# Kernel optimization log

Measured on AMD Instinct MI355X. Metric: run time of the kernel, lower is better.

Reference implementation:

```python
import jax, jax.numpy as jnp
import numpy as np


def _resize_bilinear_ac(x, Ht, Wt):
    # bilinear resize with align_corners=True; x: [B,C,h,w] -> [B,C,Ht,Wt]
    B, C, h, w = x.shape
    ys = jnp.linspace(0.0, h - 1.0, Ht)
    xs = jnp.linspace(0.0, w - 1.0, Wt)
    y0 = jnp.floor(ys).astype(jnp.int32)
    y1 = jnp.minimum(y0 + 1, h - 1)
    x0 = jnp.floor(xs).astype(jnp.int32)
    x1 = jnp.minimum(x0 + 1, w - 1)
    wy = (ys - y0).astype(x.dtype)[None, None, :, None]
    wx = (xs - x0).astype(x.dtype)[None, None, None, :]
    r0 = x[:, :, y0, :]
    r1 = x[:, :, y1, :]
    v00 = r0[:, :, :, x0]; v01 = r0[:, :, :, x1]
    v10 = r1[:, :, :, x0]; v11 = r1[:, :, :, x1]
    return (1 - wy) * ((1 - wx) * v00 + wx * v01) + wy * ((1 - wx) * v10 + wx * v11)


def _grid_sample_zeros_ac(img, grid):
    # F.grid_sample(mode='bilinear', padding_mode='zeros', align_corners=True)
    # img: [B,C,H,W], grid: [B,H,W,2] in [-1,1] (x, y)
    B, C, H, W = img.shape
    x = (grid[..., 0] + 1.0) * 0.5 * (W - 1)  # [B,H,W] pixel coords
    y = (grid[..., 1] + 1.0) * 0.5 * (H - 1)
    x0 = jnp.floor(x)
    y0 = jnp.floor(y)
    wx = (x - x0)[:, None]  # [B,1,H,W]
    wy = (y - y0)[:, None]

    def gather(xi, yi):
        valid = ((xi >= 0) & (xi <= W - 1) & (yi >= 0) & (yi <= H - 1)).astype(img.dtype)
        xc = jnp.clip(xi, 0, W - 1).astype(jnp.int32)
        yc = jnp.clip(yi, 0, H - 1).astype(jnp.int32)
        v = jax.vmap(lambda im, yy, xx: im[:, yy, xx])(img, yc, xc)  # [B,C,H,W]
        return v * valid[:, None]

    v00 = gather(x0, y0)
    v01 = gather(x0 + 1, y0)
    v10 = gather(x0, y0 + 1)
    v11 = gather(x0 + 1, y0 + 1)
    return (1 - wy) * ((1 - wx) * v00 + wx * v01) + wy * ((1 - wx) * v10 + wx * v11)


def setup_inputs() -> dict:
    key = jax.random.key(0)
    k1, k2, k3 = jax.random.split(key, 3)
    B, C, H, W = 8, 3, 384, 1280
    h, w = 96, 320
    image = jax.random.normal(k1, (B, C, H, W), dtype=jnp.float32)
    # positive disparity (fraction of width, scaled by W inside forward)
    disp = jax.random.uniform(k2, (B, 1, h, w), dtype=jnp.float32, minval=0.01, maxval=0.3)
    scene = jax.random.normal(k3, (B, 3, h, w), dtype=jnp.float32) * 0.1
    K = jnp.array([[371.0, 0.0, 320.0], [0.0, 371.0, 96.0], [0.0, 0.0, 1.0]], dtype=jnp.float32)
    intrinsic = jnp.tile(K[None], (B, 1, 1))
    aug_size = jnp.tile(jnp.array([192.0, 640.0], dtype=jnp.float32)[None], (B, 1))
    return {"image": image, "disp": disp, "scene": scene, "intrinsic": intrinsic, "aug_size": aug_size}


def reference(image, disp, scene, intrinsic, aug_size):
    B, C, H, W = image.shape
    # interpolate_as(disp, image) * W
    disp_full = _resize_bilinear_ac(disp, H, W) * W
    # rel_scale = local_scale / aug_size, local_scale = (H, W)
    rel = jnp.array([H, W], dtype=aug_size.dtype) / aug_size  # [B,2] = (sy, sx)
    sy, sx = rel[:, 0], rel[:, 1]
    fx = intrinsic[:, 0, 0] * sx
    fy = intrinsic[:, 1, 1] * sy
    cx = intrinsic[:, 0, 2] * sx
    cy = intrinsic[:, 1, 2] * sy
    z = jnp.zeros_like(fx)
    o = jnp.ones_like(fx)
    K = jnp.stack([jnp.stack([fx, z, cx], 1),
                   jnp.stack([z, fy, cy], 1),
                   jnp.stack([z, z, o], 1)], 1)  # [B,3,3]
    # disp2depth_stereo_clamp
    depth = jnp.clip(fx[:, None, None, None] * 0.54 / (disp_full + 1e-8), 0.001, 80.0)
    # pixel2point
    xg, yg = jnp.meshgrid(jnp.arange(W, dtype=jnp.float32), jnp.arange(H, dtype=jnp.float32))  # [H,W]
    pix = jnp.stack([xg.ravel(), yg.ravel(), jnp.ones(H * W, dtype=jnp.float32)], 0)  # [3,HW]
    Kinv = jnp.linalg.inv(K)
    point = jnp.einsum('bij,jn->bin', Kinv, pix) * depth.reshape(B, 1, -1)  # [B,3,HW]
    # point2pixel_ms
    scene_full = _resize_bilinear_ac(scene, H, W)
    point_form = point.reshape(B, 3, H, W) + scene_full
    proj = jnp.einsum('bij,bjn->bin', K, point_form.reshape(B, 3, -1))
    coord = (proj[:, 0:2] / (proj[:, 2:3] + 1e-8)).reshape(B, 2, H, W)
    nx = coord[:, 0] / (W - 1) * 2.0 - 1.0
    ny = coord[:, 1] / (H - 1) * 2.0 - 1.0
    grid = jnp.stack([nx, ny], -1)  # [B,H,W,2]
    return _grid_sample_zeros_ac(image, grid)
```

## Files before the change

### kernel.cpp

```cpp
#include <hip/hip_runtime.h>
#include <hip/hip_fp16.h>

#define BATCH 8
#define CH 3
#define H_OUT 384
#define W_OUT 1280
#define H_IN 96
#define W_IN 320
#define HW_OUT (H_OUT * W_OUT)
#define HW_IN (H_IN * W_IN)

#define XS_PER_ROW 20
#define YSEGS (H_OUT / 4)
#define CHUNKS_PER_B (YSEGS * XS_PER_ROW)

#define LCOLS 18
#define LROWS 3

#define P1STRIDE 1282
#define P1_HALVES ((size_t)(1 + (size_t)BATCH * H_OUT * P1STRIDE) * 4)
#define P1_BYTES (P1_HALVES * 2)

struct __attribute__((packed, aligned(4))) f2 { float x, y; };
struct __attribute__((packed, aligned(8))) h8 { unsigned int w[4]; };

static __device__ __forceinline__ __half2 u2h2(unsigned int u) {
    return *reinterpret_cast<__half2*>(&u);
}

__global__ __launch_bounds__(256) void pack_single_kernel(
    const float* __restrict__ image, __half* __restrict__ pk)
{
    int i = blockIdx.x * 256 + threadIdx.x;
    int b = i / HW_OUT;
    int p = i - b * HW_OUT;
    int y = p / W_OUT;
    int x = p - y * W_OUT;
    const float* ib = image + (size_t)b * (CH * HW_OUT) + p;
    __half2 lo = __floats2half2_rn(ib[0], ib[HW_OUT]);
    __half2 hi = __floats2half2_rn(ib[2 * HW_OUT], 0.0f);
    uint2 v;
    v.x = *reinterpret_cast<unsigned int*>(&lo);
    v.y = *reinterpret_cast<unsigned int*>(&hi);
    __half* pd = pk + 4;
    size_t row = (size_t)b * H_OUT + y;
    *reinterpret_cast<uint2*>(pd + (row * P1STRIDE + x) * 4) = v;
    if (i < BATCH * H_OUT) {
        uint2 z; z.x = 0u; z.y = 0u;
        size_t r = (size_t)i;
        *reinterpret_cast<uint2*>(pd + (r * P1STRIDE + 1280) * 4) = z;
        *reinterpret_cast<uint2*>(pd + (r * P1STRIDE + 1281) * 4) = z;
        if (i == 0) *reinterpret_cast<uint2*>(pk) = z;
    }
}

template <int MODE>
__global__ __launch_bounds__(256) void warp_sceneflow_kernel(
    const float* __restrict__ image,
    const __half* __restrict__ pk,
    const float* __restrict__ disp,
    const float* __restrict__ scene,
    const float* __restrict__ intrin,
    const float* __restrict__ aug,
    float* __restrict__ out)
{
    int bid = blockIdx.x;
    int b = bid & 7;
    int c = bid >> 3;
    int ys = c / XS_PER_ROW;
    int xs = c - ys * XS_PER_ROW;
    int ybase = ys * 4;
    int xbase = xs * 64;

    int tid = threadIdx.x;
    int wave = tid >> 6;
    int lane = tid & 63;
    int lx16 = lane & 15;
    int ly4  = lane >> 4;
    int x = xbase + wave * 16 + lx16;
    int y = ybase + ly4;

    __shared__ float4 lds4[LROWS][LCOLS];
    int ylo = (int)((float)ybase * ((float)(H_IN - 1) / (float)(H_OUT - 1)));
    int xlo = (int)((float)xbase * ((float)(W_IN - 1) / (float)(W_OUT - 1)));
    if (tid < LROWS * LCOLS) {
        int row = tid / LCOLS;
        int col = tid - row * LCOLS;
        int gy = min(ylo + row, H_IN - 1);
        int gx = min(xlo + col, W_IN - 1);
        int gi = gy * W_IN + gx;
        const float* dp = disp + b * HW_IN;
        const float* sp = scene + b * (CH * HW_IN);
        float4 v;
        v.x = dp[gi];
        v.y = sp[gi];
        v.z = sp[HW_IN + gi];
        v.w = sp[2 * HW_IN + gi];
        lds4[row][col] = v;
    }
    __syncthreads();

    float syr = (float)H_OUT / aug[b * 2 + 0];
    float sxr = (float)W_OUT / aug[b * 2 + 1];
    float fx = intrin[b * 9 + 0] * sxr;
    float fy = intrin[b * 9 + 4] * syr;
    float cx = intrin[b * 9 + 2] * sxr;
    float cy = intrin[b * 9 + 5] * syr;
    float inv_fx = 1.0f / fx;
    float inv_fy = 1.0f / fy;

    float xsrc = (float)x * ((float)(W_IN - 1) / (float)(W_OUT - 1));
    int x0 = (int)xsrc;
    float wx = xsrc - (float)x0;
    int lx = x0 - xlo;

    float ysrc = (float)y * ((float)(H_IN - 1) / (float)(H_OUT - 1));
    int y0 = (int)ysrc;
    float wy = ysrc - (float)y0;
    int ly = y0 - ylo;

    float4 t00 = lds4[ly][lx];
    float4 t01 = lds4[ly][lx + 1];
    float4 t10 = lds4[ly + 1][lx];
    float4 t11 = lds4[ly + 1][lx + 1];

    float w00 = (1.0f - wy) * (1.0f - wx);
    float w01 = (1.0f - wy) * wx;
    float w10 = wy * (1.0f - wx);
    float w11 = wy * wx;

    float dval = w00 * t00.x + w01 * t01.x + w10 * t10.x + w11 * t11.x;
    float sc0  = w00 * t00.y + w01 * t01.y + w10 * t10.y + w11 * t11.y;
    float sc1  = w00 * t00.z + w01 * t01.z + w10 * t10.z + w11 * t11.z;
    float sc2  = w00 * t00.w + w01 * t01.w + w10 * t10.w + w11 * t11.w;

    float disp_full = dval * (float)W_OUT;
    float depth = fminf(fmaxf(fx * 0.54f / (disp_full + 1e-8f), 0.001f), 80.0f);

    float X = ((float)x - cx) * inv_fx * depth + sc0;
    float Y = ((float)y - cy) * inv_fy * depth + sc1;
    float Z = depth + sc2;
    float u = fx * X + cx * Z;
    float v = fy * Y + cy * Z;
    float rw = 1.0f / (Z + 1e-8f);
    float gx = u * rw;
    float gy = v * rw;

    int ix0 = __float2int_rd(gx);
    int iy0 = __float2int_rd(gy);
    float fwx = gx - (float)ix0;
    float fwy = gy - (float)iy0;
    int ix1 = ix0 + 1, iy1 = iy0 + 1;
    bool vx0 = (ix0 >= 0) && (ix0 <= W_OUT - 1);
    bool vx1 = (ix1 >= 0) && (ix1 <= W_OUT - 1);
    bool vy0 = (iy0 >= 0) && (iy0 <= H_OUT - 1);
    bool vy1 = (iy1 >= 0) && (iy1 <= H_OUT - 1);
    float g00 = (1.0f - fwy) * (1.0f - fwx) * ((vx0 && vy0) ? 1.0f : 0.0f);
    float g01 = (1.0f - fwy) * fwx * ((vx1 && vy0) ? 1.0f : 0.0f);
    float g10 = fwy * (1.0f - fwx) * ((vx0 && vy1) ? 1.0f : 0.0f);
    float g11 = fwy * fwx * ((vx1 && vy1) ? 1.0f : 0.0f);
    int cy0 = min(max(iy0, 0), H_OUT - 1);
    int cy1 = min(max(iy1, 0), H_OUT - 1);

    float r0, r1, r2;
    if constexpr (MODE == 1) {
        int bx = min(max(ix0, -1), W_OUT - 1);
        const __half* pd = pk + 4;
        size_t rb0 = ((size_t)(b * H_OUT + cy0) * P1STRIDE + bx);
        size_t rb1 = ((size_t)(b * H_OUT + cy1) * P1STRIDE + bx);
        h8 L0 = *reinterpret_cast<const h8*>(pd + rb0 * 4);
        h8 L1 = *reinterpret_cast<const h8*>(pd + rb1 * 4);
        __half2 h0a = u2h2(L0.w[0]), h0b = u2h2(L0.w[1]);
        __half2 h1a = u2h2(L0.w[2]), h1b = u2h2(L0.w[3]);
        __half2 k0a = u2h2(L1.w[0]), k0b = u2h2(L1.w[1]);
        __half2 k1a = u2h2(L1.w[2]), k1b = u2h2(L1.w[3]);
        r0 = g00 * __low2float(h0a) + g01 * __low2float(h1a)
           + g10 * __low2float(k0a) + g11 * __low2float(k1a);
        r1 = g00 * __high2float(h0a) + g01 * __high2float(h1a)
           + g10 * __high2float(k0a) + g11 * __high2float(k1a);
        r2 = g00 * __low2float(h0b) + g01 * __low2float(h1b)
           + g10 * __low2float(k0b) + g11 * __low2float(k1b);
    } else {
        int cx0 = min(max(ix0, 0), W_OUT - 1);
        int cx1 = min(max(ix1, 0), W_OUT - 1);
        int xbi = min(cx0, W_OUT - 2);
        bool rcf = (cx0 != xbi);
        bool lcf = (cx1 == xbi);
        int rb0 = cy0 * W_OUT + xbi;
        int rb1 = cy1 * W_OUT + xbi;
        const float* ib = image + (size_t)b * (CH * HW_OUT);
        const float* im0 = ib;
        const float* im1 = ib + HW_OUT;
        const float* im2 = ib + 2 * HW_OUT;
        f2 P0 = *(const f2*)(im0 + rb0); f2 P1 = *(const f2*)(im0 + rb1);
        f2 Q0 = *(const f2*)(im1 + rb0); f2 Q1 = *(const f2*)(im1 + rb1);
        f2 T0 = *(const f2*)(im2 + rb0); f2 T1 = *(const f2*)(im2 + rb1);
        float p00 = rcf ? P0.y : P0.x, p01 = lcf ? P0.x : P0.y;
        float p10 = rcf ? P1.y : P1.x, p11 = lcf ? P1.x : P1.y;
        float q00 = rcf ? Q0.y : Q0.x, q01 = lcf ? Q0.x : Q0.y;
        float q10 = rcf ? Q1.y : Q1.x, q11 = lcf ? Q1.x : Q1.y;
        float t00f = rcf ? T0.y : T0.x, t01f = lcf ? T0.x : T0.y;
        float t10f = rcf ? T1.y : T1.x, t11f = lcf ? T1.x : T1.y;
        r0 = g00 * p00 + g01 * p01 + g10 * p10 + g11 * p11;
        r1 = g00 * q00 + g01 * q01 + g10 * q10 + g11 * q11;
        r2 = g00 * t00f + g01 * t01f + g10 * t10f + g11 * t11f;
    }

    float* ob = out + (size_t)b * (CH * HW_OUT);
    int op = y * W_OUT + x;
    __builtin_nontemporal_store(r0, ob + op);
    __builtin_nontemporal_store(r1, ob + HW_OUT + op);
    __builtin_nontemporal_store(r2, ob + 2 * HW_OUT + op);
}

extern "C" void kernel_launch(void* const* d_in, const int* in_sizes, int n_in,
                              void* d_out, int out_size, void* d_ws, size_t ws_size,
                              hipStream_t stream) {
    const float* image  = (const float*)d_in[0];
    const float* disp   = (const float*)d_in[1];
    const float* scene  = (const float*)d_in[2];
    const float* intrin = (const float*)d_in[3];
    const float* aug    = (const float*)d_in[4];
    float* out = (float*)d_out;

    const int grid = BATCH * CHUNKS_PER_B;

    if (ws_size >= P1_BYTES) {
        __half* pk = (__half*)d_ws;
        pack_single_kernel<<<BATCH * HW_OUT / 256, 256, 0, stream>>>(image, pk);
        warp_sceneflow_kernel<1><<<grid, 256, 0, stream>>>(
            image, pk, disp, scene, intrin, aug, out);
    } else {
        warp_sceneflow_kernel<0><<<grid, 256, 0, stream>>>(
            image, nullptr, disp, scene, intrin, aug, out);
    }
}
```

Before: 52.12 us.

## Vectorize image packing and switch warp kernel to square 16x16 tiles

Result: slower. 56.45 us (+8.3%).

```diff
diff --git a/kernel.cpp b/kernel.cpp
--- a/kernel.cpp
+++ b/kernel.cpp
@@ -10,12 +10,12 @@
 #define HW_OUT (H_OUT * W_OUT)
 #define HW_IN (H_IN * W_IN)
 
-#define XS_PER_ROW 20
-#define YSEGS (H_OUT / 4)
+#define XS_PER_ROW (W_OUT / 16)
+#define YSEGS (H_OUT / 16)
 #define CHUNKS_PER_B (YSEGS * XS_PER_ROW)
 
-#define LCOLS 18
-#define LROWS 3
+#define LCOLS 6
+#define LROWS 6
 
 #define P1STRIDE 1282
 #define P1_HALVES ((size_t)(1 + (size_t)BATCH * H_OUT * P1STRIDE) * 4)
@@ -23,34 +23,54 @@
 
 struct __attribute__((packed, aligned(4))) f2 { float x, y; };
 struct __attribute__((packed, aligned(8))) h8 { unsigned int w[4]; };
+struct __attribute__((packed, aligned(8))) u4 { unsigned int w[4]; };
+
+typedef float vf4 __attribute__((ext_vector_type(4)));
 
 static __device__ __forceinline__ __half2 u2h2(unsigned int u) {
     return *reinterpret_cast<__half2*>(&u);
+}
+static __device__ __forceinline__ unsigned int h2u(__half2 h) {
+    return *reinterpret_cast<unsigned int*>(&h);
 }
 
 __global__ __launch_bounds__(256) void pack_single_kernel(
     const float* __restrict__ image, __half* __restrict__ pk)
 {
-    int i = blockIdx.x * 256 + threadIdx.x;
-    int b = i / HW_OUT;
-    int p = i - b * HW_OUT;
+    int bid = blockIdx.x;
+    int b = bid & 7;
+    int chunk = bid >> 3;
+    int p = chunk * 1024 + threadIdx.x * 4;
     int y = p / W_OUT;
     int x = p - y * W_OUT;
+
     const float* ib = image + (size_t)b * (CH * HW_OUT) + p;
-    __half2 lo = __floats2half2_rn(ib[0], ib[HW_OUT]);
-    __half2 hi = __floats2half2_rn(ib[2 * HW_OUT], 0.0f);
-    uint2 v;
-    v.x = *reinterpret_cast<unsigned int*>(&lo);
-    v.y = *reinterpret_cast<unsigned int*>(&hi);
+    vf4 A  = __builtin_nontemporal_load(reinterpret_cast<const vf4*>(ib));
+    vf4 Bv = __builtin_nontemporal_load(reinterpret_cast<const vf4*>(ib + HW_OUT));
+    vf4 Cv = __builtin_nontemporal_load(reinterpret_cast<const vf4*>(ib + 2 * HW_OUT));
+
+    u4 s0, s1;
+    s0.w[0] = h2u(__floats2half2_rn(A.x, Bv.x));
+    s0.w[1] = h2u(__floats2half2_rn(Cv.x, 0.0f));
+    s0.w[2] = h2u(__floats2half2_rn(A.y, Bv.y));
+    s0.w[3] = h2u(__floats2half2_rn(Cv.y, 0.0f));
+    s1.w[0] = h2u(__floats2half2_rn(A.z, Bv.z));
+    s1.w[1] = h2u(__floats2half2_rn(Cv.z, 0.0f));
+    s1.w[2] = h2u(__floats2half2_rn(A.w, Bv.w));
+    s1.w[3] = h2u(__floats2half2_rn(Cv.w, 0.0f));
+
     __half* pd = pk + 4;
-    size_t row = (size_t)b * H_OUT + y;
-    *reinterpret_cast<uint2*>(pd + (row * P1STRIDE + x) * 4) = v;
-    if (i < BATCH * H_OUT) {
+    size_t off = ((size_t)(b * H_OUT + y) * P1STRIDE + x) * 4;
+    *reinterpret_cast<u4*>(pd + off) = s0;
+    *reinterpret_cast<u4*>(pd + off + 8) = s1;
+
+    int gt = bid * 256 + threadIdx.x;
+    if (gt < BATCH * H_OUT) {
         uint2 z; z.x = 0u; z.y = 0u;
-        size_t r = (size_t)i;
+        size_t r = (size_t)gt;
         *reinterpret_cast<uint2*>(pd + (r * P1STRIDE + 1280) * 4) = z;
         *reinterpret_cast<uint2*>(pd + (r * P1STRIDE + 1281) * 4) = z;
-        if (i == 0) *reinterpret_cast<uint2*>(pk) = z;
+        if (gt == 0) *reinterpret_cast<uint2*>(pk) = z;
     }
 }
 
@@ -69,16 +89,14 @@
     int c = bid >> 3;
     int ys = c / XS_PER_ROW;
     int xs = c - ys * XS_PER_ROW;
-    int ybase = ys * 4;
-    int xbase = xs * 64;
+    int ybase = ys * 16;
+    int xbase = xs * 16;
 
     int tid = threadIdx.x;
     int wave = tid >> 6;
     int lane = tid & 63;
-    int lx16 = lane & 15;
-    int ly4  = lane >> 4;
-    int x = xbase + wave * 16 + lx16;
-    int y = ybase + ly4;
+    int x = xbase + ((wave & 1) << 3) + (lane & 7);
+    int y = ybase + ((wave >> 1) << 3) + (lane >> 3);
 
     __shared__ float4 lds4[LROWS][LCOLS];
     int ylo = (int)((float)ybase * ((float)(H_IN - 1) / (float)(H_OUT - 1)));
@@ -227,7 +245,7 @@
 
     if (ws_size >= P1_BYTES) {
         __half* pk = (__half*)d_ws;
-        pack_single_kernel<<<BATCH * HW_OUT / 256, 256, 0, stream>>>(image, pk);
+        pack_single_kernel<<<BATCH * HW_OUT / 1024, 256, 0, stream>>>(image, pk);
         warp_sceneflow_kernel<1><<<grid, 256, 0, stream>>>(
             image, pk, disp, scene, intrin, aug, out);
     } else {
```
